# Kernel optimization log

Hardware: AMD Instinct MI355X
Metric: run time of the kernel (lower is better)

Reference implementation:

```python
import jax, jax.numpy as jnp
import numpy as np


def setup_inputs() -> dict:
    key = jax.random.key(0)
    k1, k2, k3, k4, k5 = jax.random.split(key, 5)
    B, T, H = 32, 4096, 256
    D = 2 * H  # encoder feature dim
    hidden = jax.random.normal(k1, (B, D), dtype=jnp.float32)
    encoder_outputs = jax.random.normal(k2, (B, T, D), dtype=jnp.float32)
    # torch nn.Linear(4H, H): weight [H, 4H], bias [H]
    W_attn = jax.random.normal(k3, (H, 4 * H), dtype=jnp.float32) * (1.0 / np.sqrt(4 * H))
    b_attn = jax.random.normal(k4, (H,), dtype=jnp.float32) * 0.01
    v = jax.random.uniform(k5, (H,), dtype=jnp.float32)  # torch.rand init
    return {"hidden": hidden, "encoder_outputs": encoder_outputs,
            "W_attn": W_attn, "b_attn": b_attn, "v": v}


def reference(hidden, encoder_outputs, W_attn, b_attn, v):
    D = hidden.shape[-1]  # 2*H
    # Split Linear(4H->H) weight into the hidden part and encoder part so we
    # never materialize the [B,T,4H] concat: cat(h,e) @ W.T == h @ Wh.T + e @ We.T
    W_h = W_attn[:, :D]   # [H, 2H]
    W_e = W_attn[:, D:]   # [H, 2H]
    h_proj = hidden @ W_h.T                     # [B, H]
    e_proj = jnp.einsum('btd,hd->bth', encoder_outputs, W_e)  # [B, T, H]
    energy = jnp.tanh(h_proj[:, None, :] + e_proj + b_attn)   # [B, T, H]
    scores = energy @ v                          # [B, T]
    attn_weights = jax.nn.softmax(scores, axis=1)  # softmax over timesteps
    context = jnp.einsum('bt,btd->bd', attn_weights, encoder_outputs)  # [B, 2H]
    return context, attn_weights
```

## Files before the change

### kernel.cpp

```cpp
#include <hip/hip_runtime.h>
#include <math.h>

#define B_  32
#define T_  4096
#define H_  256
#define D_  512

#define WS_PRE    0
#define WS_WEHI   32768
#define WS_P      294912
#define WS_ML     819200
#define WS_PCTX   827392

using short8  = __attribute__((ext_vector_type(8))) short;
using float4v = __attribute__((ext_vector_type(4))) float;

__device__ __forceinline__ unsigned short f32_to_bf16_rne(float x) {
    unsigned u = __float_as_uint(x);
    unsigned r = u + 0x7fffu + ((u >> 16) & 1u);
    return (unsigned short)(r >> 16);
}

__global__ __launch_bounds__(256)
void prep_kernel(const float* __restrict__ hidden,
                 const float* __restrict__ W_attn,
                 const float* __restrict__ b_attn,
                 unsigned char* __restrict__ ws) {
    int blk = blockIdx.x;
    int tid = threadIdx.x;
    if (blk < 32) {
        int b = blk, h = tid;
        const float4* hv = (const float4*)(hidden + b * D_);
        const float4* wv = (const float4*)(W_attn + (size_t)h * 1024);
        float s = 0.f;
        #pragma unroll 4
        for (int d4 = 0; d4 < D_ / 4; ++d4) {
            float4 a = hv[d4], w = wv[d4];
            s += a.x * w.x + a.y * w.y + a.z * w.z + a.w * w.w;
        }
        ((float*)(ws + WS_PRE))[b * H_ + h] = s + b_attn[h];
    } else {
        int base = (blk - 32) * 16384 + tid;
        unsigned short* whi = (unsigned short*)(ws + WS_WEHI);
        #pragma unroll 4
        for (int i = 0; i < 64; ++i) {
            int idx = base + i * 256;
            int n = idx >> 9, k = idx & 511;
            whi[idx] = f32_to_bf16_rne(W_attn[(size_t)n * 1024 + 512 + k]);
        }
    }
}

#define BM 128
#define BN 256
#define BK 32
#define LDT 40

__global__ __launch_bounds__(512, 4)
void gemm_scores_kernel(const float* __restrict__ enc,
                        unsigned char* __restrict__ ws,
                        const float* __restrict__ v) {
    __shared__ unsigned short sA[2][BM * LDT];
    __shared__ unsigned short sB[2][BN * LDT];
    __shared__ float sScore[BM];
    __shared__ float sP[BM];
    __shared__ float sRed[4];

    const float*          pre = (const float*)(ws + WS_PRE);
    const unsigned short* weh = (const unsigned short*)(ws + WS_WEHI);

    int tid = threadIdx.x;
    int m0  = blockIdx.x * BM;
    int b   = m0 >> 12;

    if (tid < BM) sScore[tid] = 0.f;

    int rowA = tid & 127, cgA = tid >> 7;
    const float* gA = enc + (size_t)(m0 + rowA) * D_ + cgA * 8;
    int rowB = tid >> 1, hB = tid & 1;
    const unsigned short* gB = weh + (size_t)rowB * D_ + hB * 16;

    int wave = tid >> 6, lane = tid & 63;
    int wm = wave & 1, wn = wave >> 1;
    int quad = lane >> 4, l16 = lane & 15;

    float4v acc[4][4] = {};

    float a_reg[8];
    uint4 br0, br1;

    {
        const float4* p = (const float4*)gA;
        *(float4*)(a_reg)     = p[0];
        *(float4*)(a_reg + 4) = p[1];
        br0 = ((const uint4*)gB)[0]; br1 = ((const uint4*)gB)[1];

        unsigned short hi8[8];
        #pragma unroll
        for (int j = 0; j < 8; ++j) hi8[j] = f32_to_bf16_rne(a_reg[j]);
        *(short8*)&sA[0][rowA * LDT + cgA * 8] = *(short8*)hi8;
        *(uint4*)&sB[0][rowB * LDT + hB * 16]     = br0;
        *(uint4*)&sB[0][rowB * LDT + hB * 16 + 8] = br1;

        const float4* p1 = (const float4*)(gA + BK);
        *(float4*)(a_reg)     = p1[0];
        *(float4*)(a_reg + 4) = p1[1];
        const uint4* pb1 = (const uint4*)(gB + BK);
        br0 = pb1[0]; br1 = pb1[1];
    }
    __builtin_amdgcn_s_waitcnt(0xc07f);
    __builtin_amdgcn_s_barrier();

    const int KIT = D_ / BK;
    for (int kk = 0; kk < KIT; ++kk) {
        int cur = kk & 1, nxt = cur ^ 1;

        short8 ah[4], bh[4];
        #pragma unroll
        for (int i = 0; i < 4; ++i) {
            int r = wm * 64 + i * 16 + l16;
            ah[i] = *(const short8*)&sA[cur][r * LDT + quad * 8];
        }
        #pragma unroll
        for (int j = 0; j < 4; ++j) {
            int c = wn * 64 + j * 16 + l16;
            bh[j] = *(const short8*)&sB[cur][c * LDT + quad * 8];
        }

        if (kk + 1 < KIT) {
            unsigned short hi8[8];
            #pragma unroll
            for (int j = 0; j < 8; ++j) hi8[j] = f32_to_bf16_rne(a_reg[j]);
            *(short8*)&sA[nxt][rowA * LDT + cgA * 8] = *(short8*)hi8;
            *(uint4*)&sB[nxt][rowB * LDT + hB * 16]     = br0;
            *(uint4*)&sB[nxt][rowB * LDT + hB * 16 + 8] = br1;
        }
        if (kk + 2 < KIT) {
            const float4* p = (const float4*)(gA + (kk + 2) * BK);
            *(float4*)(a_reg)     = p[0];
            *(float4*)(a_reg + 4) = p[1];
            const uint4* pb = (const uint4*)(gB + (kk + 2) * BK);
            br0 = pb[0]; br1 = pb[1];
        }

        #pragma unroll
        for (int i = 0; i < 4; ++i)
            #pragma unroll
            for (int j = 0; j < 4; ++j)
                acc[i][j] = __builtin_amdgcn_mfma_f32_16x16x32_bf16(ah[i], bh[j], acc[i][j], 0, 0, 0);

        if (kk + 1 < KIT) {
            __builtin_amdgcn_s_waitcnt(0xc07f);
            __builtin_amdgcn_s_barrier();
        }
    }

    float rowsum[4][4] = {};
    #pragma unroll
    for (int j = 0; j < 4; ++j) {
        int n = wn * 64 + j * 16 + l16;
        float pv = pre[b * H_ + n];
        float vv = v[n];
        #pragma unroll
        for (int i = 0; i < 4; ++i)
            #pragma unroll
            for (int r = 0; r < 4; ++r)
                rowsum[i][r] += tanhf(acc[i][j][r] + pv) * vv;
    }
    #pragma unroll
    for (int i = 0; i < 4; ++i)
        #pragma unroll
        for (int r = 0; r < 4; ++r) {
            float s = rowsum[i][r];
            s += __shfl_xor(s, 1);
            s += __shfl_xor(s, 2);
            s += __shfl_xor(s, 4);
            s += __shfl_xor(s, 8);
            rowsum[i][r] = s;
        }
    if (l16 == 0) {
        #pragma unroll
        for (int i = 0; i < 4; ++i)
            #pragma unroll
            for (int r = 0; r < 4; ++r) {
                int row = wm * 64 + i * 16 + quad * 4 + r;
                atomicAdd(&sScore[row], rowsum[i][r]);
            }
    }
    __syncthreads();

    if (tid < 128) {
        float s = sScore[tid];
        float m = s;
        #pragma unroll
        for (int off = 32; off; off >>= 1) m = fmaxf(m, __shfl_xor(m, off));
        if (lane == 0) sRed[wave] = m;
    }
    __syncthreads();
    float m_blk = fmaxf(sRed[0], sRed[1]);
    if (tid < 128) {
        float p = expf(sScore[tid] - m_blk);
        sP[tid] = p;
        ((float*)(ws + WS_P))[m0 + tid] = p;
        float l = p;
        #pragma unroll
        for (int off = 32; off; off >>= 1) l += __shfl_xor(l, off);
        if (lane == 0) sRed[2 + wave] = l;
    }
    __syncthreads();
    if (tid == 0) {
        float2 ml = make_float2(m_blk, sRed[2] + sRed[3]);
        ((float2*)(ws + WS_ML))[blockIdx.x] = ml;
    }

    int colg = tid & 127, rgrp = tid >> 7;
    const float* encb = enc + (size_t)m0 * D_;
    float4 c4 = {0.f, 0.f, 0.f, 0.f};
    #pragma unroll 4
    for (int s = 0; s < 32; ++s) {
        int r = rgrp + 4 * s;
        float w = sP[r];
        float4 ev = *(const float4*)(encb + (size_t)r * D_ + colg * 4);
        c4.x += w * ev.x; c4.y += w * ev.y;
        c4.z += w * ev.z; c4.w += w * ev.w;
    }
    float4* red4 = (float4*)sA;
    red4[tid] = c4;
    __syncthreads();
    if (rgrp == 0) {
        float4 a0 = red4[colg], a1 = red4[colg + 128];
        float4 a2 = red4[colg + 256], a3 = red4[colg + 384];
        float4 o;
        o.x = a0.x + a1.x + a2.x + a3.x;
        o.y = a0.y + a1.y + a2.y + a3.y;
        o.z = a0.z + a1.z + a2.z + a3.z;
        o.w = a0.w + a1.w + a2.w + a3.w;
        ((float4*)(ws + WS_PCTX))[blockIdx.x * 128 + colg] = o;
    }
}

__global__ __launch_bounds__(512)
void finalize_kernel(const unsigned char* __restrict__ ws,
                     float* __restrict__ out_ctx,
                     float* __restrict__ out_w) {
    __shared__ float sm[32], sl[32], sscale[32];
    int b = blockIdx.x, tid = threadIdx.x;
    const float2* ml  = ((const float2*)(ws + WS_ML)) + b * 32;
    if (tid < 32) {
        float2 v = ml[tid];
        sm[tid] = v.x; sl[tid] = v.y;
    }
    __syncthreads();
    float m = -1e30f;
    #pragma unroll
    for (int i = 0; i < 32; ++i) m = fmaxf(m, sm[i]);
    float l = 0.f;
    #pragma unroll
    for (int i = 0; i < 32; ++i) l += sl[i] * expf(sm[i] - m);
    float inv = 1.0f / l;
    if (tid < 32) sscale[tid] = expf(sm[tid] - m) * inv;
    __syncthreads();

    {
        const float4* pb = (const float4*)((const float*)(ws + WS_P) + (size_t)b * T_);
        float4* wb = (float4*)(out_w + (size_t)b * T_);
        int t0 = tid * 2;
        float sc = sscale[tid >> 4];
        float4 x = pb[t0], y = pb[t0 + 1];
        x.x *= sc; x.y *= sc; x.z *= sc; x.w *= sc;
        y.x *= sc; y.y *= sc; y.z *= sc; y.w *= sc;
        wb[t0] = x; wb[t0 + 1] = y;
    }
    {
        const float* pc = (const float*)(ws + WS_PCTX) + (size_t)b * 32 * D_;
        float c = 0.f;
        #pragma unroll
        for (int i = 0; i < 32; ++i) c += pc[i * D_ + tid] * sscale[i];
        out_ctx[b * D_ + tid] = c;
    }
}

extern "C" void kernel_launch(void* const* d_in, const int* in_sizes, int n_in,
                              void* d_out, int out_size, void* d_ws, size_t ws_size,
                              hipStream_t stream) {
    const float* hidden = (const float*)d_in[0];
    const float* enc    = (const float*)d_in[1];
    const float* W_attn = (const float*)d_in[2];
    const float* b_attn = (const float*)d_in[3];
    const float* v      = (const float*)d_in[4];
    float* out = (float*)d_out;
    unsigned char* ws = (unsigned char*)d_ws;

    prep_kernel<<<40, 256, 0, stream>>>(hidden, W_attn, b_attn, ws);
    gemm_scores_kernel<<<T_ * B_ / BM, 512, 0, stream>>>(enc, ws, v);
    finalize_kernel<<<B_, 512, 0, stream>>>(ws, out, out + B_ * D_);
}
```

Before: 439.3 us.

## Pre-swizzle bf16 weight tiles, use packed bf16 conversion and fast tanh

The prep kernel now writes the encoder-part weights in a K-tile-major, XOR-swizzled bf16 layout, so the GEMM can copy B tiles to shared memory with contiguous 16-byte loads and read them without padding or bank conflicts. Activation conversion switches to packed float2-to-bf16 intrinsics. The main loop alternates between two register buffers and defers the shared-memory stores until after the MFMAs. tanhf is replaced by an exp/rcp approximation, which gives up a little accuracy to cut the cost of the epilogue.

Measured after the change: 421.4 us. 1.04x faster.

```diff
diff --git a/kernel.cpp b/kernel.cpp
--- a/kernel.cpp
+++ b/kernel.cpp
@@ -1,4 +1,5 @@
 #include <hip/hip_runtime.h>
+#include <hip/hip_bf16.h>
 #include <math.h>
 
 #define B_  32
@@ -15,10 +16,23 @@
 using short8  = __attribute__((ext_vector_type(8))) short;
 using float4v = __attribute__((ext_vector_type(4))) float;
 
-__device__ __forceinline__ unsigned short f32_to_bf16_rne(float x) {
-    unsigned u = __float_as_uint(x);
-    unsigned r = u + 0x7fffu + ((u >> 16) & 1u);
-    return (unsigned short)(r >> 16);
+__device__ __forceinline__ unsigned cvt2_bf16(float lo, float hi) {
+    union { __hip_bfloat162 h; unsigned u; } cv;
+    cv.h = __float22bfloat162_rn(make_float2(lo, hi));
+    return cv.u;
+}
+__device__ __forceinline__ short8 cvt8_bf16(const float* a) {
+    union { unsigned u[4]; short8 s; } r;
+    r.u[0] = cvt2_bf16(a[0], a[1]);
+    r.u[1] = cvt2_bf16(a[2], a[3]);
+    r.u[2] = cvt2_bf16(a[4], a[5]);
+    r.u[3] = cvt2_bf16(a[6], a[7]);
+    return r.s;
+}
+
+__device__ __forceinline__ float fast_tanh(float x) {
+    float e = __expf(2.0f * x);
+    return 1.0f - 2.0f * __builtin_amdgcn_rcpf(e + 1.0f);
 }
 
 __global__ __launch_bounds__(256)
@@ -40,13 +54,20 @@
         }
         ((float*)(ws + WS_PRE))[b * H_ + h] = s + b_attn[h];
     } else {
-        int base = (blk - 32) * 16384 + tid;
+        int q = (blk - 32) * 256 + tid;
         unsigned short* whi = (unsigned short*)(ws + WS_WEHI);
-        #pragma unroll 4
-        for (int i = 0; i < 64; ++i) {
-            int idx = base + i * 256;
-            int n = idx >> 9, k = idx & 511;
-            whi[idx] = f32_to_bf16_rne(W_attn[(size_t)n * 1024 + 512 + k]);
+        #pragma unroll
+        for (int i = 0; i < 4; ++i) {
+            int idx4 = q + i * 8192;
+            int n = idx4 >> 7, k = (idx4 & 127) << 2;
+            int t = k >> 5, kin = k & 31;
+            int quad = kin >> 3, e = kin & 7;
+            int slot = quad ^ ((n >> 1) & 3);
+            float4 w = *(const float4*)(W_attn + (size_t)n * 1024 + 512 + k);
+            unsigned lo = cvt2_bf16(w.x, w.y);
+            unsigned hi = cvt2_bf16(w.z, w.w);
+            unsigned short* dst = whi + t * 8192 + n * 32 + slot * 8 + e;
+            *(uint2*)dst = make_uint2(lo, hi);
         }
     }
 }
@@ -55,13 +76,14 @@
 #define BN 256
 #define BK 32
 #define LDT 40
+#define KIT 16
 
 __global__ __launch_bounds__(512, 4)
 void gemm_scores_kernel(const float* __restrict__ enc,
                         unsigned char* __restrict__ ws,
                         const float* __restrict__ v) {
     __shared__ unsigned short sA[2][BM * LDT];
-    __shared__ unsigned short sB[2][BN * LDT];
+    __shared__ unsigned short sB[2][BN * BK];
     __shared__ float sScore[BM];
     __shared__ float sP[BM];
     __shared__ float sRed[4];
@@ -77,8 +99,6 @@
 
     int rowA = tid & 127, cgA = tid >> 7;
     const float* gA = enc + (size_t)(m0 + rowA) * D_ + cgA * 8;
-    int rowB = tid >> 1, hB = tid & 1;
-    const unsigned short* gB = weh + (size_t)rowB * D_ + hB * 16;
 
     int wave = tid >> 6, lane = tid & 63;
     int wm = wave & 1, wn = wave >> 1;
@@ -86,74 +106,69 @@
 
     float4v acc[4][4] = {};
 
-    float a_reg[8];
-    uint4 br0, br1;
+    float aX[8], aY[8];
 
     {
-        const float4* p = (const float4*)gA;
-        *(float4*)(a_reg)     = p[0];
-        *(float4*)(a_reg + 4) = p[1];
-        br0 = ((const uint4*)gB)[0]; br1 = ((const uint4*)gB)[1];
-
-        unsigned short hi8[8];
-        #pragma unroll
-        for (int j = 0; j < 8; ++j) hi8[j] = f32_to_bf16_rne(a_reg[j]);
-        *(short8*)&sA[0][rowA * LDT + cgA * 8] = *(short8*)hi8;
-        *(uint4*)&sB[0][rowB * LDT + hB * 16]     = br0;
-        *(uint4*)&sB[0][rowB * LDT + hB * 16 + 8] = br1;
-
+        const float4* p0 = (const float4*)gA;
+        float4 x0 = p0[0], x1 = p0[1];
+        const uint4* pb0 = (const uint4*)weh;
+        uint4 t0 = pb0[tid], t1 = pb0[tid + 512];
         const float4* p1 = (const float4*)(gA + BK);
-        *(float4*)(a_reg)     = p1[0];
-        *(float4*)(a_reg + 4) = p1[1];
-        const uint4* pb1 = (const uint4*)(gB + BK);
-        br0 = pb1[0]; br1 = pb1[1];
+        float4 y0 = p1[0], y1 = p1[1];
+
+        float tmp[8];
+        *(float4*)tmp = x0; *(float4*)(tmp + 4) = x1;
+        *(short8*)&sA[0][rowA * LDT + cgA * 8] = cvt8_bf16(tmp);
+        ((uint4*)sB[0])[tid]       = t0;
+        ((uint4*)sB[0])[tid + 512] = t1;
+        *(float4*)aY = y0; *(float4*)(aY + 4) = y1;
     }
     __builtin_amdgcn_s_waitcnt(0xc07f);
     __builtin_amdgcn_s_barrier();
 
-    const int KIT = D_ / BK;
-    for (int kk = 0; kk < KIT; ++kk) {
-        int cur = kk & 1, nxt = cur ^ 1;
-
-        short8 ah[4], bh[4];
-        #pragma unroll
-        for (int i = 0; i < 4; ++i) {
-            int r = wm * 64 + i * 16 + l16;
-            ah[i] = *(const short8*)&sA[cur][r * LDT + quad * 8];
-        }
-        #pragma unroll
-        for (int j = 0; j < 4; ++j) {
-            int c = wn * 64 + j * 16 + l16;
-            bh[j] = *(const short8*)&sB[cur][c * LDT + quad * 8];
-        }
-
-        if (kk + 1 < KIT) {
-            unsigned short hi8[8];
-            #pragma unroll
-            for (int j = 0; j < 8; ++j) hi8[j] = f32_to_bf16_rne(a_reg[j]);
-            *(short8*)&sA[nxt][rowA * LDT + cgA * 8] = *(short8*)hi8;
-            *(uint4*)&sB[nxt][rowB * LDT + hB * 16]     = br0;
-            *(uint4*)&sB[nxt][rowB * LDT + hB * 16 + 8] = br1;
-        }
-        if (kk + 2 < KIT) {
-            const float4* p = (const float4*)(gA + (kk + 2) * BK);
-            *(float4*)(a_reg)     = p[0];
-            *(float4*)(a_reg + 4) = p[1];
-            const uint4* pb = (const uint4*)(gB + (kk + 2) * BK);
-            br0 = pb[0]; br1 = pb[1];
-        }
-
-        #pragma unroll
-        for (int i = 0; i < 4; ++i)
-            #pragma unroll
-            for (int j = 0; j < 4; ++j)
-                acc[i][j] = __builtin_amdgcn_mfma_f32_16x16x32_bf16(ah[i], bh[j], acc[i][j], 0, 0, 0);
-
-        if (kk + 1 < KIT) {
-            __builtin_amdgcn_s_waitcnt(0xc07f);
-            __builtin_amdgcn_s_barrier();
-        }
-    }
+#define K_STEP(kk, CUR, NXT, Acons, Aload)                                    \
+    {                                                                         \
+        uint4 br0, br1;                                                       \
+        if ((kk) + 1 < KIT) {                                                 \
+            const uint4* pb = (const uint4*)(weh + ((kk) + 1) * 8192);        \
+            br0 = pb[tid]; br1 = pb[tid + 512];                               \
+        }                                                                     \
+        if ((kk) + 2 < KIT) {                                                 \
+            const float4* pa = (const float4*)(gA + ((kk) + 2) * BK);         \
+            *(float4*)(Aload) = pa[0]; *(float4*)((Aload) + 4) = pa[1];       \
+        }                                                                     \
+        short8 ah[4], bh[4];                                                  \
+        _Pragma("unroll")                                                     \
+        for (int i = 0; i < 4; ++i) {                                         \
+            int r = wm * 64 + i * 16 + l16;                                   \
+            ah[i] = *(const short8*)&sA[CUR][r * LDT + quad * 8];             \
+        }                                                                     \
+        _Pragma("unroll")                                                     \
+        for (int j = 0; j < 4; ++j) {                                         \
+            int c = wn * 64 + j * 16 + l16;                                   \
+            int slot = quad ^ ((c >> 1) & 3);                                 \
+            bh[j] = *(const short8*)&sB[CUR][c * 32 + slot * 8];              \
+        }                                                                     \
+        _Pragma("unroll")                                                     \
+        for (int i = 0; i < 4; ++i)                                           \
+            _Pragma("unroll")                                                 \
+            for (int j = 0; j < 4; ++j)                                       \
+                acc[i][j] = __builtin_amdgcn_mfma_f32_16x16x32_bf16(          \
+                    ah[i], bh[j], acc[i][j], 0, 0, 0);                        \
+        if ((kk) + 1 < KIT) {                                                 \
+            *(short8*)&sA[NXT][rowA * LDT + cgA * 8] = cvt8_bf16(Acons);      \
+            ((uint4*)sB[NXT])[tid]       = br0;                               \
+            ((uint4*)sB[NXT])[tid + 512] = br1;                               \
+            __builtin_amdgcn_s_waitcnt(0xc07f);                               \
+            __builtin_amdgcn_s_barrier();                                     \
+        }                                                                     \
+    }
+
+    for (int kt = 0; kt < 8; ++kt) {
+        K_STEP(2 * kt,     0, 1, aY, aX)
+        K_STEP(2 * kt + 1, 1, 0, aX, aY)
+    }
+#undef K_STEP
 
     float rowsum[4][4] = {};
     #pragma unroll
@@ -165,7 +180,7 @@
         for (int i = 0; i < 4; ++i)
             #pragma unroll
             for (int r = 0; r < 4; ++r)
-                rowsum[i][r] += tanhf(acc[i][j][r] + pv) * vv;
+                rowsum[i][r] += fast_tanh(acc[i][j][r] + pv) * vv;
     }
     #pragma unroll
     for (int i = 0; i < 4; ++i)
@@ -291,7 +306,7 @@
     float* out = (float*)d_out;
     unsigned char* ws = (unsigned char*)d_ws;
 
-    prep_kernel<<<40, 256, 0, stream>>>(hidden, W_attn, b_attn, ws);
+    prep_kernel<<<64, 256, 0, stream>>>(hidden, W_attn, b_attn, ws);
     gemm_scores_kernel<<<T_ * B_ / BM, 512, 0, stream>>>(enc, ws, v);
     finalize_kernel<<<B_, 512, 0, stream>>>(ws, out, out + B_ * D_);
 }
```
